# Performance work log

Measured on AMD Instinct MI355X. Metric: run time of the kernel, lower is better.

Reference implementation:

```python
import jax, jax.numpy as jnp
import numpy as np

LN_EPS = 1e-3  # keras LayerNormalization default epsilon


def _layernorm(x, gamma, beta):
    mu = jnp.mean(x, axis=-1, keepdims=True)
    var = jnp.mean(jnp.square(x - mu), axis=-1, keepdims=True)
    return (x - mu) * jax.lax.rsqrt(var + LN_EPS) * gamma + beta


def setup_inputs() -> dict:
    key = jax.random.key(0)
    ks = jax.random.split(key, 8)
    B, H, W, C = 4, 64, 64, 256
    units = 256
    s = 1.0 / np.sqrt(C)  # he-normal-ish scale for 1x1 convs
    return {
        "inputs": jax.random.normal(ks[0], (B, H, W, C), jnp.float32),
        "context": jax.random.normal(ks[1], (B, H, W, C), jnp.float32),
        "Wq": jax.random.normal(ks[2], (C, units), jnp.float32) * s,
        "bq": jnp.zeros((units,), jnp.float32),
        "Wk": jax.random.normal(ks[3], (C, units), jnp.float32) * s,
        "bk": jnp.zeros((units,), jnp.float32),
        "Wv": jax.random.normal(ks[4], (C, units), jnp.float32) * s,
        "bv": jnp.zeros((units,), jnp.float32),
        "Wp": jax.random.normal(ks[5], (units, units), jnp.float32) * s,
        "bp": jnp.zeros((units,), jnp.float32),
        "gamma": jnp.ones((C,), jnp.float32),
        "beta": jnp.zeros((C,), jnp.float32),
    }


def reference(inputs, context, Wq, bq, Wk, bk, Wv, bv, Wp, bp, gamma, beta):
    B, H, W, C = inputs.shape
    units = Wq.shape[1]
    scale = jnp.float32(units) ** -0.5

    x_n = _layernorm(inputs, gamma, beta)          # normalized inputs (also residual base)
    q = jnp.einsum('bhwc,cu->bhwu', x_n, Wq) + bq   # [B,H,W,U]
    k = jnp.einsum('bhwc,cu->bhwu', context, Wk) + bk
    v = jnp.einsum('bhwc,cu->bhwu', context, Wv) + bv

    # full (h*w) x (H*W) score tensor, as in the original
    scores = jnp.einsum('bhwc,bHWc->bhwHW', q, k) * scale
    scores = scores.reshape(B, H, W, H * W)
    attn = jax.nn.softmax(scores, axis=-1).reshape(B, H, W, H, W)

    out = jnp.einsum('bhwHW,bHWc->bhwc', attn, v)
    proj = jnp.einsum('bhwc,cu->bhwu', out, Wp) + bp
    return x_n + proj
```

## Files before the change

kernel.cpp:

```cpp
#include <hip/hip_runtime.h>

typedef short v8s __attribute__((ext_vector_type(8)));
typedef float v4f __attribute__((ext_vector_type(4)));
using u16 = unsigned short;

#define QSCALE 0.09016844f

__device__ __forceinline__ u16 f2b(float f) {
  union { float f; unsigned u; } v; v.f = f;
  unsigned r = v.u + 0x7FFFu + ((v.u >> 16) & 1u);
  return (u16)(r >> 16);
}

__global__ void ln_prep(const float* __restrict__ x, const float* __restrict__ ctx,
                        const float* __restrict__ gamma, const float* __restrict__ beta,
                        float* __restrict__ xn_f, u16* __restrict__ xn_b,
                        u16* __restrict__ ctx_b)
{
  const int tid = threadIdx.x;
  const int wid = tid >> 6, lane = tid & 63;
  const int row = blockIdx.x * 4 + wid;
  const size_t tidx = ((size_t)(row >> 4) * 8 + (lane >> 3)) * 512 +
                      (((lane >> 1) & 3) * 16 + (row & 15)) * 8 + (lane & 1) * 4;
  if (blockIdx.y == 0) {
    const float4 xv = *(const float4*)(x + (size_t)row * 256 + lane * 4);
    float s1 = xv.x + xv.y + xv.z + xv.w;
    float s2 = xv.x*xv.x + xv.y*xv.y + xv.z*xv.z + xv.w*xv.w;
#pragma unroll
    for (int m = 32; m >= 1; m >>= 1) {
      s1 += __shfl_xor(s1, m);
      s2 += __shfl_xor(s2, m);
    }
    const float mu  = s1 * (1.0f/256.0f);
    const float var = s2 * (1.0f/256.0f) - mu*mu;
    const float rs  = rsqrtf(var + 1e-3f);
    const float4 g = *(const float4*)(gamma + lane*4);
    const float4 b = *(const float4*)(beta  + lane*4);
    float4 y;
    y.x = (xv.x-mu)*rs*g.x + b.x;
    y.y = (xv.y-mu)*rs*g.y + b.y;
    y.z = (xv.z-mu)*rs*g.z + b.z;
    y.w = (xv.w-mu)*rs*g.w + b.w;
    *(float4*)(xn_f + (size_t)row*256 + lane*4) = y;
    ushort4 yb; yb.x=f2b(y.x); yb.y=f2b(y.y); yb.z=f2b(y.z); yb.w=f2b(y.w);
    *(ushort4*)(xn_b + tidx) = yb;
  } else {
    const float4 cv = *(const float4*)(ctx + (size_t)row * 256 + lane * 4);
    ushort4 cb; cb.x=f2b(cv.x); cb.y=f2b(cv.y); cb.z=f2b(cv.z); cb.w=f2b(cv.w);
    *(ushort4*)(ctx_b + tidx) = cb;
  }
}

__global__ void wtrans(const float* __restrict__ wq, const float* __restrict__ wk,
                       const float* __restrict__ wv, const float* __restrict__ wp,
                       u16* __restrict__ tq, u16* __restrict__ tk,
                       u16* __restrict__ tv, u16* __restrict__ tp)
{
  const float* src; u16* dst; float scl = 1.0f;
  switch (blockIdx.y) {
    case 0:  src = wq; dst = tq; scl = QSCALE; break;
    case 1:  src = wk; dst = tk; break;
    case 2:  src = wv; dst = tv; break;
    default: src = wp; dst = tp; break;
  }
  const int t  = threadIdx.x;
  const int kk = blockIdx.x * 16 + (t >> 4);
  const int n0 = (t & 15) * 16;
  const size_t base = (size_t)((t & 15) * 8 + (kk >> 5)) * 512 +
                      ((kk >> 3) & 3) * 16 * 8 + (kk & 7);
#pragma unroll
  for (int j = 0; j < 16; j++)
    dst[base + (size_t)j * 8] = f2b(src[(size_t)kk * 256 + n0 + j] * scl);
}

__global__ __launch_bounds__(256) void gemm_qkv(
    const u16* __restrict__ xn_b, const u16* __restrict__ ctx_b,
    const u16* __restrict__ wqt, const u16* __restrict__ wkt, const u16* __restrict__ wvt,
    const float* __restrict__ bq, const float* __restrict__ bk, const float* __restrict__ bv,
    u16* __restrict__ qo, u16* __restrict__ ko, u16* __restrict__ vto)
{
  const int mode = blockIdx.y;
  const u16* A; const u16* Wt; const float* bias;
  if (mode == 0)      { A = xn_b;  Wt = wqt; bias = bq; }
  else if (mode == 1) { A = ctx_b; Wt = wkt; bias = bk; }
  else                { A = ctx_b; Wt = wvt; bias = bv; }
  const float bscale = (mode == 0) ? QSCALE : 1.0f;
  const int wid = threadIdx.x >> 6, lane = threadIdx.x & 63;
  const int lm = lane & 15, q4 = lane >> 4;
  const int m0 = blockIdx.x * 64 + wid * 16;
  const u16* abase = A + (size_t)(m0 >> 4) * 4096 + lane * 8;
  v8s af[8];
#pragma unroll
  for (int kf = 0; kf < 8; kf++) af[kf] = *(const v8s*)(abase + kf * 512);
#pragma unroll
  for (int ct = 0; ct < 16; ct++) {
    const int c = ct * 16 + lm;
    const u16* wbase = Wt + (size_t)ct * 4096 + lane * 8;
    v8s wf[8];
#pragma unroll
    for (int kf = 0; kf < 8; kf++) wf[kf] = *(const v8s*)(wbase + kf * 512);
    v4f a0 = {0.f,0.f,0.f,0.f}, a1 = a0, a2 = a0, a3 = a0;
    a0 = __builtin_amdgcn_mfma_f32_16x16x32_bf16(af[0], wf[0], a0, 0, 0, 0);
    a1 = __builtin_amdgcn_mfma_f32_16x16x32_bf16(af[2], wf[2], a1, 0, 0, 0);
    a2 = __builtin_amdgcn_mfma_f32_16x16x32_bf16(af[4], wf[4], a2, 0, 0, 0);
    a3 = __builtin_amdgcn_mfma_f32_16x16x32_bf16(af[6], wf[6], a3, 0, 0, 0);
    a0 = __builtin_amdgcn_mfma_f32_16x16x32_bf16(af[1], wf[1], a0, 0, 0, 0);
    a1 = __builtin_amdgcn_mfma_f32_16x16x32_bf16(af[3], wf[3], a1, 0, 0, 0);
    a2 = __builtin_amdgcn_mfma_f32_16x16x32_bf16(af[5], wf[5], a2, 0, 0, 0);
    a3 = __builtin_amdgcn_mfma_f32_16x16x32_bf16(af[7], wf[7], a3, 0, 0, 0);
    const v4f acc = (a0 + a1) + (a2 + a3);
    const float bb = bias[c] * bscale;
    if (mode == 2) {
      const int b = m0 >> 12;
      const int chunk = (m0 & 4095) >> 6;
      const int kic = (m0 & 63) + q4 * 4;
      const int ks = kic >> 5;
      const int q4p = (kic >> 3) & 3;
      const size_t idx = ((size_t)(b * 64 + chunk) * 32 + (c >> 4) * 2 + ks) * 512 +
                         (q4p * 16 + (c & 15)) * 8 + (q4 & 1) * 4;
      ushort4 pk;
      pk.x = f2b(acc[0] + bb); pk.y = f2b(acc[1] + bb);
      pk.z = f2b(acc[2] + bb); pk.w = f2b(acc[3] + bb);
      *(ushort4*)(vto + idx) = pk;
    } else {
      u16* out = (mode == 0) ? qo : ko;
      const size_t base = ((size_t)(m0 >> 4) * 8 + (c >> 5)) * 512 +
                          (((c >> 3) & 3) * 16 + q4 * 4) * 8 + (c & 7);
#pragma unroll
      for (int r = 0; r < 4; r++)
        out[base + (size_t)r * 8] = f2b(acc[r] + bb);
    }
  }
}

__global__ __launch_bounds__(512, 2) void attn_kernel(
    const u16* __restrict__ q, const u16* __restrict__ k,
    const u16* __restrict__ vt, u16* __restrict__ ao)
{
  __shared__ u16 P[2][64][136];
  __shared__ float Lp[8][64];
  __shared__ float Lt[64];
  const int bid  = blockIdx.x;
  const int b    = (bid & 7) >> 1;
  const int qblk = ((bid >> 3) << 1) | (bid & 1);
  const int tid  = threadIdx.x;
  const int w    = tid >> 6, lane = tid & 63;
  const int lm   = lane & 15, q4 = lane >> 4;
  const int m0   = qblk * 64;
  const u16* qb = q  + (size_t)b * 1048576;
  const u16* kb = k  + (size_t)b * 1048576;
  const u16* vb = vt + (size_t)b * 1048576;

  v8s qf[4][8];
#pragma unroll
  for (int qt = 0; qt < 4; qt++) {
    const u16* qbase = qb + (size_t)((m0 >> 4) + qt) * 4096 + lane * 8;
#pragma unroll
    for (int kf = 0; kf < 8; kf++) qf[qt][kf] = *(const v8s*)(qbase + kf * 512);
  }

  v4f o[4][2];
#pragma unroll
  for (int qt = 0; qt < 4; qt++)
#pragma unroll
    for (int ct = 0; ct < 2; ct++) o[qt][ct] = (v4f){0.f, 0.f, 0.f, 0.f};
  float lsum[4] = {0.f, 0.f, 0.f, 0.f};

  v8s kfr[8];
  {
    const u16* kbase = kb + (size_t)w * 4096 + lane * 8;
#pragma unroll
    for (int kf = 0; kf < 8; kf++) kfr[kf] = *(const v8s*)(kbase + kf * 512);
  }

  for (int c128 = 0; c128 < 32; c128++) {
    const int pb = c128 & 1;
    v8s vfr[2][4];
#pragma unroll
    for (int ct = 0; ct < 2; ct++)
#pragma unroll
      for (int j = 0; j < 4; j++) {
        const size_t tile = (size_t)(c128 * 2 + (j >> 1)) * 32 +
                            (w * 2 + ct) * 2 + (j & 1);
        vfr[ct][j] = *(const v8s*)(vb + tile * 512 + lane * 8);
      }
    v4f sc[4];
#pragma unroll
    for (int qt = 0; qt < 4; qt++) sc[qt] = (v4f){0.f, 0.f, 0.f, 0.f};
#pragma unroll
    for (int kf = 0; kf < 8; kf++)
#pragma unroll
      for (int qt = 0; qt < 4; qt++)
        sc[qt] = __builtin_amdgcn_mfma_f32_16x16x32_bf16(kfr[kf], qf[qt][kf], sc[qt], 0, 0, 0);
    {
      const int nc = (c128 + 1) & 31;
      const u16* kbase = kb + (size_t)(nc * 8 + w) * 4096 + lane * 8;
#pragma unroll
      for (int kf = 0; kf < 8; kf++) kfr[kf] = *(const v8s*)(kbase + kf * 512);
    }
#pragma unroll
    for (int qt = 0; qt < 4; qt++) {
      const float e0 = exp2f(sc[qt][0]);
      const float e1 = exp2f(sc[qt][1]);
      const float e2 = exp2f(sc[qt][2]);
      const float e3 = exp2f(sc[qt][3]);
      lsum[qt] += (e0 + e1) + (e2 + e3);
      unsigned d0, d1;
      asm("v_cvt_pk_bf16_f32 %0, %1, %2" : "=v"(d0) : "v"(e0), "v"(e1));
      asm("v_cvt_pk_bf16_f32 %0, %1, %2" : "=v"(d1) : "v"(e2), "v"(e3));
      uint2 pk; pk.x = d0; pk.y = d1;
      *(uint2*)(&P[pb][qt * 16 + lm][w * 16 + q4 * 4]) = pk;
    }
    __syncthreads();
#pragma unroll
    for (int qt = 0; qt < 4; qt++) {
      v8s pf[4];
#pragma unroll
      for (int j = 0; j < 4; j++)
        pf[j] = *(const v8s*)(&P[pb][qt * 16 + lm][j * 32 + q4 * 8]);
#pragma unroll
      for (int ct = 0; ct < 2; ct++)
#pragma unroll
        for (int j = 0; j < 4; j++)
          o[qt][ct] = __builtin_amdgcn_mfma_f32_16x16x32_bf16(pf[j], vfr[ct][j], o[qt][ct], 0, 0, 0);
    }
  }

#pragma unroll
  for (int qt = 0; qt < 4; qt++) {
    float t = lsum[qt];
    t += __shfl_xor(t, 16);
    t += __shfl_xor(t, 32);
    lsum[qt] = t;
  }
  if (q4 == 0) {
#pragma unroll
    for (int qt = 0; qt < 4; qt++) Lp[w][qt * 16 + lm] = lsum[qt];
  }
  __syncthreads();
  if (tid < 64) {
    float t = 0.f;
#pragma unroll
    for (int ww = 0; ww < 8; ww++) t += Lp[ww][tid];
    Lt[tid] = t;
  }
  __syncthreads();

  const int rstrip0 = (b * 4096 + m0) >> 4;
#pragma unroll
  for (int qt = 0; qt < 4; qt++)
#pragma unroll
    for (int r = 0; r < 4; r++) {
      const float linv = 1.0f / Lt[qt * 16 + q4 * 4 + r];
#pragma unroll
      for (int ct = 0; ct < 2; ct++) {
        const int ch = w * 32 + ct * 16 + lm;
        const size_t idx = ((size_t)(rstrip0 + qt) * 8 + (ch >> 5)) * 512 +
                           (((ch >> 3) & 3) * 16 + q4 * 4 + r) * 8 + (ch & 7);
        ao[idx] = f2b(o[qt][ct][r] * linv);
      }
    }
}

__global__ __launch_bounds__(256) void gemm_proj(
    const u16* __restrict__ A, const u16* __restrict__ Wt, const float* __restrict__ bias,
    const float* __restrict__ xn_f, float* __restrict__ out)
{
  const int wid = threadIdx.x >> 6, lane = threadIdx.x & 63;
  const int lm = lane & 15, q4 = lane >> 4;
  const int m0 = blockIdx.x * 64 + wid * 16;
  const u16* abase = A + (size_t)(m0 >> 4) * 4096 + lane * 8;
  v8s af[8];
#pragma unroll
  for (int kf = 0; kf < 8; kf++) af[kf] = *(const v8s*)(abase + kf * 512);
#pragma unroll
  for (int ct = 0; ct < 16; ct++) {
    const int c = ct * 16 + lm;
    const u16* wbase = Wt + (size_t)ct * 4096 + lane * 8;
    v8s wf[8];
#pragma unroll
    for (int kf = 0; kf < 8; kf++) wf[kf] = *(const v8s*)(wbase + kf * 512);
    v4f a0 = {0.f,0.f,0.f,0.f}, a1 = a0, a2 = a0, a3 = a0;
    a0 = __builtin_amdgcn_mfma_f32_16x16x32_bf16(af[0], wf[0], a0, 0, 0, 0);
    a1 = __builtin_amdgcn_mfma_f32_16x16x32_bf16(af[2], wf[2], a1, 0, 0, 0);
    a2 = __builtin_amdgcn_mfma_f32_16x16x32_bf16(af[4], wf[4], a2, 0, 0, 0);
    a3 = __builtin_amdgcn_mfma_f32_16x16x32_bf16(af[6], wf[6], a3, 0, 0, 0);
    a0 = __builtin_amdgcn_mfma_f32_16x16x32_bf16(af[1], wf[1], a0, 0, 0, 0);
    a1 = __builtin_amdgcn_mfma_f32_16x16x32_bf16(af[3], wf[3], a1, 0, 0, 0);
    a2 = __builtin_amdgcn_mfma_f32_16x16x32_bf16(af[5], wf[5], a2, 0, 0, 0);
    a3 = __builtin_amdgcn_mfma_f32_16x16x32_bf16(af[7], wf[7], a3, 0, 0, 0);
    const v4f acc = (a0 + a1) + (a2 + a3);
    const float bb = bias[c];
#pragma unroll
    for (int r = 0; r < 4; r++) {
      const size_t idx = (size_t)(m0 + q4 * 4 + r) * 256 + c;
      out[idx] = xn_f[idx] + acc[r] + bb;
    }
  }
}

extern "C" void kernel_launch(void* const* d_in, const int* in_sizes, int n_in,
                              void* d_out, int out_size, void* d_ws, size_t ws_size,
                              hipStream_t stream)
{
  (void)in_sizes; (void)n_in; (void)out_size; (void)ws_size;
  const float* inputs  = (const float*)d_in[0];
  const float* context = (const float*)d_in[1];
  const float* Wq = (const float*)d_in[2];
  const float* bq = (const float*)d_in[3];
  const float* Wk = (const float*)d_in[4];
  const float* bk = (const float*)d_in[5];
  const float* Wv = (const float*)d_in[6];
  const float* bv = (const float*)d_in[7];
  const float* Wp = (const float*)d_in[8];
  const float* bp = (const float*)d_in[9];
  const float* gamma = (const float*)d_in[10];
  const float* beta  = (const float*)d_in[11];
  float* out = (float*)d_out;

  char* p = (char*)d_ws;
  float* xn_f = (float*)p; p += (size_t)16384 * 256 * 4;
  u16* xn_b   = (u16*)p;   p += (size_t)16384 * 256 * 2;
  u16* ctx_b  = (u16*)p;   p += (size_t)16384 * 256 * 2;
  u16* qbuf   = (u16*)p;   p += (size_t)16384 * 256 * 2;
  u16* kbuf   = (u16*)p;   p += (size_t)16384 * 256 * 2;
  u16* vtbuf  = (u16*)p;   p += (size_t)16384 * 256 * 2;
  u16* wqt = (u16*)p; p += (size_t)256 * 256 * 2;
  u16* wkt = (u16*)p; p += (size_t)256 * 256 * 2;
  u16* wvt = (u16*)p; p += (size_t)256 * 256 * 2;
  u16* wpt = (u16*)p; p += (size_t)256 * 256 * 2;
  u16* aobuf = xn_b;

  ln_prep<<<dim3(4096, 2), 256, 0, stream>>>(inputs, context, gamma, beta, xn_f, xn_b, ctx_b);
  wtrans<<<dim3(16, 4), 256, 0, stream>>>(Wq, Wk, Wv, Wp, wqt, wkt, wvt, wpt);
  gemm_qkv<<<dim3(256, 3), 256, 0, stream>>>(xn_b, ctx_b, wqt, wkt, wvt, bq, bk, bv, qbuf, kbuf, vtbuf);
  attn_kernel<<<dim3(256), 512, 0, stream>>>(qbuf, kbuf, vtbuf, aobuf);
  gemm_proj<<<dim3(256), 256, 0, stream>>>(aobuf, wpt, bp, xn_f, out);
}
```

Baseline: 216.7 us.

## Split attention key range across two blocks and merge partials in projection

Each query block's 4096 keys are now split into two halves handled by separate workgroups, doubling the attention grid to 512 blocks. Each half writes a normalized partial output plus its row sums, and the projection GEMM reweights and merges the two partials before the matmul. Launch bounds go from 2 to 4 waves per SIMD to let more blocks co-reside. The aim is better CU occupancy on a grid that previously had only 256 blocks. The cost is extra partial-output traffic, an extra bf16 rounding of the merged output, and possible register pressure or spilling from the tighter launch bound.

```diff
diff --git a/kernel.cpp b/kernel.cpp
--- a/kernel.cpp
+++ b/kernel.cpp
@@ -10,6 +10,10 @@
   union { float f; unsigned u; } v; v.f = f;
   unsigned r = v.u + 0x7FFFu + ((v.u >> 16) & 1u);
   return (u16)(r >> 16);
+}
+__device__ __forceinline__ float b2f(u16 h) {
+  union { unsigned u; float f; } v; v.u = ((unsigned)h) << 16;
+  return v.f;
 }
 
 __global__ void ln_prep(const float* __restrict__ x, const float* __restrict__ ctx,
@@ -133,16 +137,18 @@
   }
 }
 
-__global__ __launch_bounds__(512, 2) void attn_kernel(
+__global__ __launch_bounds__(512, 4) void attn_kernel(
     const u16* __restrict__ q, const u16* __restrict__ k,
-    const u16* __restrict__ vt, u16* __restrict__ ao)
+    const u16* __restrict__ vt, u16* __restrict__ o0, u16* __restrict__ o1,
+    float* __restrict__ Lq)
 {
   __shared__ u16 P[2][64][136];
   __shared__ float Lp[8][64];
   __shared__ float Lt[64];
   const int bid  = blockIdx.x;
   const int b    = (bid & 7) >> 1;
-  const int qblk = ((bid >> 3) << 1) | (bid & 1);
+  const int ks   = bid & 1;
+  const int qblk = bid >> 3;
   const int tid  = threadIdx.x;
   const int w    = tid >> 6, lane = tid & 63;
   const int lm   = lane & 15, q4 = lane >> 4;
@@ -150,6 +156,7 @@
   const u16* qb = q  + (size_t)b * 1048576;
   const u16* kb = k  + (size_t)b * 1048576;
   const u16* vb = vt + (size_t)b * 1048576;
+  const int c0 = ks * 16;
 
   v8s qf[4][8];
 #pragma unroll
@@ -168,12 +175,12 @@
 
   v8s kfr[8];
   {
-    const u16* kbase = kb + (size_t)w * 4096 + lane * 8;
+    const u16* kbase = kb + (size_t)(c0 * 8 + w) * 4096 + lane * 8;
 #pragma unroll
     for (int kf = 0; kf < 8; kf++) kfr[kf] = *(const v8s*)(kbase + kf * 512);
   }
 
-  for (int c128 = 0; c128 < 32; c128++) {
+  for (int c128 = c0; c128 < c0 + 16; c128++) {
     const int pb = c128 & 1;
     v8s vfr[2][4];
 #pragma unroll
@@ -193,7 +200,7 @@
       for (int qt = 0; qt < 4; qt++)
         sc[qt] = __builtin_amdgcn_mfma_f32_16x16x32_bf16(kfr[kf], qf[qt][kf], sc[qt], 0, 0, 0);
     {
-      const int nc = (c128 + 1) & 31;
+      const int nc = c0 + ((c128 + 1 - c0) & 15);
       const u16* kbase = kb + (size_t)(nc * 8 + w) * 4096 + lane * 8;
 #pragma unroll
       for (int kf = 0; kf < 8; kf++) kfr[kf] = *(const v8s*)(kbase + kf * 512);
@@ -243,9 +250,11 @@
 #pragma unroll
     for (int ww = 0; ww < 8; ww++) t += Lp[ww][tid];
     Lt[tid] = t;
+    Lq[ks * 16384 + b * 4096 + m0 + tid] = t;
   }
   __syncthreads();
 
+  u16* od = ks ? o1 : o0;
   const int rstrip0 = (b * 4096 + m0) >> 4;
 #pragma unroll
   for (int qt = 0; qt < 4; qt++)
@@ -257,22 +266,39 @@
         const int ch = w * 32 + ct * 16 + lm;
         const size_t idx = ((size_t)(rstrip0 + qt) * 8 + (ch >> 5)) * 512 +
                            (((ch >> 3) & 3) * 16 + q4 * 4 + r) * 8 + (ch & 7);
-        ao[idx] = f2b(o[qt][ct][r] * linv);
+        od[idx] = f2b(o[qt][ct][r] * linv);
       }
     }
 }
 
 __global__ __launch_bounds__(256) void gemm_proj(
-    const u16* __restrict__ A, const u16* __restrict__ Wt, const float* __restrict__ bias,
+    const u16* __restrict__ o0, const u16* __restrict__ o1,
+    const float* __restrict__ Lq,
+    const u16* __restrict__ Wt, const float* __restrict__ bias,
     const float* __restrict__ xn_f, float* __restrict__ out)
 {
   const int wid = threadIdx.x >> 6, lane = threadIdx.x & 63;
   const int lm = lane & 15, q4 = lane >> 4;
   const int m0 = blockIdx.x * 64 + wid * 16;
-  const u16* abase = A + (size_t)(m0 >> 4) * 4096 + lane * 8;
+  const float l0 = Lq[m0 + lm];
+  const float l1 = Lq[16384 + m0 + lm];
+  const float w0 = l0 / (l0 + l1);
+  const float w1 = 1.0f - w0;
+  const u16* a0base = o0 + (size_t)(m0 >> 4) * 4096 + lane * 8;
+  const u16* a1base = o1 + (size_t)(m0 >> 4) * 4096 + lane * 8;
   v8s af[8];
 #pragma unroll
-  for (int kf = 0; kf < 8; kf++) af[kf] = *(const v8s*)(abase + kf * 512);
+  for (int kf = 0; kf < 8; kf++) {
+    const v8s x0 = *(const v8s*)(a0base + kf * 512);
+    const v8s x1 = *(const v8s*)(a1base + kf * 512);
+    v8s m;
+#pragma unroll
+    for (int e = 0; e < 8; e++) {
+      const float f = w0 * b2f((u16)x0[e]) + w1 * b2f((u16)x1[e]);
+      m[e] = (short)f2b(f);
+    }
+    af[kf] = m;
+  }
 #pragma unroll
   for (int ct = 0; ct < 16; ct++) {
     const int c = ct * 16 + lm;
@@ -329,11 +355,13 @@
   u16* wkt = (u16*)p; p += (size_t)256 * 256 * 2;
   u16* wvt = (u16*)p; p += (size_t)256 * 256 * 2;
   u16* wpt = (u16*)p; p += (size_t)256 * 256 * 2;
-  u16* aobuf = xn_b;
+  float* Lq = (float*)p; p += (size_t)2 * 16384 * 4;
+  u16* o0 = xn_b;
+  u16* o1 = ctx_b;
 
   ln_prep<<<dim3(4096, 2), 256, 0, stream>>>(inputs, context, gamma, beta, xn_f, xn_b, ctx_b);
   wtrans<<<dim3(16, 4), 256, 0, stream>>>(Wq, Wk, Wv, Wp, wqt, wkt, wvt, wpt);
   gemm_qkv<<<dim3(256, 3), 256, 0, stream>>>(xn_b, ctx_b, wqt, wkt, wvt, bq, bk, bv, qbuf, kbuf, vtbuf);
-  attn_kernel<<<dim3(256), 512, 0, stream>>>(qbuf, kbuf, vtbuf, aobuf);
-  gemm_proj<<<dim3(256), 256, 0, stream>>>(aobuf, wpt, bp, xn_f, out);
-}
+  attn_kernel<<<dim3(512), 512, 0, stream>>>(qbuf, kbuf, vtbuf, o0, o1, Lq);
+  gemm_proj<<<dim3(256), 256, 0, stream>>>(o0, o1, Lq, wpt, bp, xn_f, out);
+}
```

After: 504.1 us. 2.33x slower.

## Stage epilogue outputs through LDS for coalesced vector global stores

Applied to the files above, without the earlier changes.

The layernorm/convert kernel now processes 16 rows per block and writes the tiled bf16 layout through a shared-memory buffer, so global stores are 16-byte vectors. The QKV GEMM and the projection GEMM likewise stage their output tiles in LDS and then write them out contiguously. The projection GEMM also reads the residual with float4 loads and uses a swizzle against bank conflicts. This replaces scattered 2-byte and 4-byte global stores, at the cost of extra LDS traffic, a barrier, and larger shared memory (64KB in gemm_proj) that can reduce occupancy.

```diff
diff --git a/kernel.cpp b/kernel.cpp
--- a/kernel.cpp
+++ b/kernel.cpp
@@ -12,42 +12,61 @@
   return (u16)(r >> 16);
 }
 
-__global__ void ln_prep(const float* __restrict__ x, const float* __restrict__ ctx,
-                        const float* __restrict__ gamma, const float* __restrict__ beta,
-                        float* __restrict__ xn_f, u16* __restrict__ xn_b,
-                        u16* __restrict__ ctx_b)
-{
+__global__ __launch_bounds__(256) void ln_prep(
+    const float* __restrict__ x, const float* __restrict__ ctx,
+    const float* __restrict__ gamma, const float* __restrict__ beta,
+    float* __restrict__ xn_f, u16* __restrict__ xn_b, u16* __restrict__ ctx_b)
+{
+  __shared__ u16 Y[16][264];
   const int tid = threadIdx.x;
-  const int wid = tid >> 6, lane = tid & 63;
-  const int row = blockIdx.x * 4 + wid;
-  const size_t tidx = ((size_t)(row >> 4) * 8 + (lane >> 3)) * 512 +
-                      (((lane >> 1) & 3) * 16 + (row & 15)) * 8 + (lane & 1) * 4;
+  const int w = tid >> 6, lane = tid & 63;
+  const int rowg0 = blockIdx.x * 16;
   if (blockIdx.y == 0) {
-    const float4 xv = *(const float4*)(x + (size_t)row * 256 + lane * 4);
-    float s1 = xv.x + xv.y + xv.z + xv.w;
-    float s2 = xv.x*xv.x + xv.y*xv.y + xv.z*xv.z + xv.w*xv.w;
-#pragma unroll
-    for (int m = 32; m >= 1; m >>= 1) {
-      s1 += __shfl_xor(s1, m);
-      s2 += __shfl_xor(s2, m);
-    }
-    const float mu  = s1 * (1.0f/256.0f);
-    const float var = s2 * (1.0f/256.0f) - mu*mu;
-    const float rs  = rsqrtf(var + 1e-3f);
     const float4 g = *(const float4*)(gamma + lane*4);
     const float4 b = *(const float4*)(beta  + lane*4);
-    float4 y;
-    y.x = (xv.x-mu)*rs*g.x + b.x;
-    y.y = (xv.y-mu)*rs*g.y + b.y;
-    y.z = (xv.z-mu)*rs*g.z + b.z;
-    y.w = (xv.w-mu)*rs*g.w + b.w;
-    *(float4*)(xn_f + (size_t)row*256 + lane*4) = y;
-    ushort4 yb; yb.x=f2b(y.x); yb.y=f2b(y.y); yb.z=f2b(y.z); yb.w=f2b(y.w);
-    *(ushort4*)(xn_b + tidx) = yb;
+#pragma unroll
+    for (int rr = 0; rr < 4; rr++) {
+      const int r16 = w * 4 + rr;
+      const int row = rowg0 + r16;
+      const float4 xv = *(const float4*)(x + (size_t)row * 256 + lane * 4);
+      float s1 = xv.x + xv.y + xv.z + xv.w;
+      float s2 = xv.x*xv.x + xv.y*xv.y + xv.z*xv.z + xv.w*xv.w;
+#pragma unroll
+      for (int m = 32; m >= 1; m >>= 1) {
+        s1 += __shfl_xor(s1, m);
+        s2 += __shfl_xor(s2, m);
+      }
+      const float mu  = s1 * (1.0f/256.0f);
+      const float var = s2 * (1.0f/256.0f) - mu*mu;
+      const float rs  = rsqrtf(var + 1e-3f);
+      float4 y;
+      y.x = (xv.x-mu)*rs*g.x + b.x;
+      y.y = (xv.y-mu)*rs*g.y + b.y;
+      y.z = (xv.z-mu)*rs*g.z + b.z;
+      y.w = (xv.w-mu)*rs*g.w + b.w;
+      *(float4*)(xn_f + (size_t)row*256 + lane*4) = y;
+      ushort4 yb; yb.x=f2b(y.x); yb.y=f2b(y.y); yb.z=f2b(y.z); yb.w=f2b(y.w);
+      *(ushort4*)(&Y[r16][lane*4]) = yb;
+    }
   } else {
-    const float4 cv = *(const float4*)(ctx + (size_t)row * 256 + lane * 4);
-    ushort4 cb; cb.x=f2b(cv.x); cb.y=f2b(cv.y); cb.z=f2b(cv.z); cb.w=f2b(cv.w);
-    *(ushort4*)(ctx_b + tidx) = cb;
+#pragma unroll
+    for (int rr = 0; rr < 4; rr++) {
+      const int r16 = w * 4 + rr;
+      const int row = rowg0 + r16;
+      const float4 cv = *(const float4*)(ctx + (size_t)row * 256 + lane * 4);
+      ushort4 cb; cb.x=f2b(cv.x); cb.y=f2b(cv.y); cb.z=f2b(cv.z); cb.w=f2b(cv.w);
+      *(ushort4*)(&Y[r16][lane*4]) = cb;
+    }
+  }
+  __syncthreads();
+  u16* dst = (blockIdx.y == 0 ? xn_b : ctx_b) + (size_t)blockIdx.x * 4096;
+#pragma unroll
+  for (int j = 0; j < 2; j++) {
+    const int o8  = tid + j * 256;
+    const int sub = o8 >> 6, within = o8 & 63;
+    const int row = within & 15, chq = within >> 4;
+    const int ch  = sub * 32 + chq * 8;
+    *(v8s*)(dst + (size_t)o8 * 8) = *(const v8s*)(&Y[row][ch]);
   }
 }
 
@@ -79,6 +98,7 @@
     const float* __restrict__ bq, const float* __restrict__ bk, const float* __restrict__ bv,
     u16* __restrict__ qo, u16* __restrict__ ko, u16* __restrict__ vto)
 {
+  __shared__ u16 Cb[16384];
   const int mode = blockIdx.y;
   const u16* A; const u16* Wt; const float* bias;
   if (mode == 0)      { A = xn_b;  Wt = wqt; bias = bq; }
@@ -87,7 +107,8 @@
   const float bscale = (mode == 0) ? QSCALE : 1.0f;
   const int wid = threadIdx.x >> 6, lane = threadIdx.x & 63;
   const int lm = lane & 15, q4 = lane >> 4;
-  const int m0 = blockIdx.x * 64 + wid * 16;
+  const int m0b = blockIdx.x * 64;
+  const int m0 = m0b + wid * 16;
   const u16* abase = A + (size_t)(m0 >> 4) * 4096 + lane * 8;
   v8s af[8];
 #pragma unroll
@@ -111,25 +132,33 @@
     const v4f acc = (a0 + a1) + (a2 + a3);
     const float bb = bias[c] * bscale;
     if (mode == 2) {
-      const int b = m0 >> 12;
-      const int chunk = (m0 & 4095) >> 6;
       const int kic = (m0 & 63) + q4 * 4;
-      const int ks = kic >> 5;
+      const int ks  = kic >> 5;
       const int q4p = (kic >> 3) & 3;
-      const size_t idx = ((size_t)(b * 64 + chunk) * 32 + (c >> 4) * 2 + ks) * 512 +
-                         (q4p * 16 + (c & 15)) * 8 + (q4 & 1) * 4;
+      const int lidx = ((c >> 4) * 2 + ks) * 512 + (q4p * 16 + (c & 15)) * 8 + (q4 & 1) * 4;
       ushort4 pk;
       pk.x = f2b(acc[0] + bb); pk.y = f2b(acc[1] + bb);
       pk.z = f2b(acc[2] + bb); pk.w = f2b(acc[3] + bb);
-      *(ushort4*)(vto + idx) = pk;
+      *(ushort4*)(&Cb[lidx]) = pk;
     } else {
-      u16* out = (mode == 0) ? qo : ko;
-      const size_t base = ((size_t)(m0 >> 4) * 8 + (c >> 5)) * 512 +
-                          (((c >> 3) & 3) * 16 + q4 * 4) * 8 + (c & 7);
-#pragma unroll
-      for (int r = 0; r < 4; r++)
-        out[base + (size_t)r * 8] = f2b(acc[r] + bb);
-    }
+      const int lidx = wid * 4096 + (c >> 5) * 512 +
+                       (((c >> 3) & 3) * 16 + q4 * 4) * 8 + (c & 7);
+#pragma unroll
+      for (int r = 0; r < 4; r++) Cb[lidx + r * 8] = f2b(acc[r] + bb);
+    }
+  }
+  __syncthreads();
+  u16* gdst;
+  if (mode == 2) {
+    const int b = m0b >> 12, chunk = (m0b & 4095) >> 6;
+    gdst = vto + (size_t)(b * 64 + chunk) * 16384;
+  } else {
+    gdst = (mode == 0 ? qo : ko) + (size_t)(m0b >> 4) * 4096;
+  }
+#pragma unroll
+  for (int j = 0; j < 8; j++) {
+    const int o8 = threadIdx.x + j * 256;
+    *(v8s*)(gdst + (size_t)o8 * 8) = *(const v8s*)(&Cb[o8 * 8]);
   }
 }
 
@@ -266,9 +295,11 @@
     const u16* __restrict__ A, const u16* __restrict__ Wt, const float* __restrict__ bias,
     const float* __restrict__ xn_f, float* __restrict__ out)
 {
+  __shared__ float Cf[64][256];
   const int wid = threadIdx.x >> 6, lane = threadIdx.x & 63;
   const int lm = lane & 15, q4 = lane >> 4;
-  const int m0 = blockIdx.x * 64 + wid * 16;
+  const int m0b = blockIdx.x * 64;
+  const int m0 = m0b + wid * 16;
   const u16* abase = A + (size_t)(m0 >> 4) * 4096 + lane * 8;
   v8s af[8];
 #pragma unroll
@@ -293,9 +324,25 @@
     const float bb = bias[c];
 #pragma unroll
     for (int r = 0; r < 4; r++) {
-      const size_t idx = (size_t)(m0 + q4 * 4 + r) * 256 + c;
-      out[idx] = xn_f[idx] + acc[r] + bb;
-    }
+      const int row = wid * 16 + q4 * 4 + r;
+      Cf[row][c ^ (q4 * 8)] = acc[r] + bb;
+    }
+  }
+  __syncthreads();
+  const float* xb = xn_f + (size_t)m0b * 256;
+  float* ob = out + (size_t)m0b * 256;
+#pragma unroll
+  for (int j = 0; j < 16; j++) {
+    const int u = threadIdx.x + j * 256;
+    const int row = u >> 6;
+    const int c = (u & 63) * 4;
+    const int csw = c ^ (((row >> 2) & 3) * 8);
+    const float4 a4 = *(const float4*)(&Cf[row][csw]);
+    const float4 x4 = *(const float4*)(xb + (size_t)row * 256 + c);
+    float4 o4;
+    o4.x = a4.x + x4.x; o4.y = a4.y + x4.y;
+    o4.z = a4.z + x4.z; o4.w = a4.w + x4.w;
+    *(float4*)(ob + (size_t)row * 256 + c) = o4;
   }
 }
 
@@ -331,7 +378,7 @@
   u16* wpt = (u16*)p; p += (size_t)256 * 256 * 2;
   u16* aobuf = xn_b;
 
-  ln_prep<<<dim3(4096, 2), 256, 0, stream>>>(inputs, context, gamma, beta, xn_f, xn_b, ctx_b);
+  ln_prep<<<dim3(1024, 2), 256, 0, stream>>>(inputs, context, gamma, beta, xn_f, xn_b, ctx_b);
   wtrans<<<dim3(16, 4), 256, 0, stream>>>(Wq, Wk, Wv, Wp, wqt, wkt, wvt, wpt);
   gemm_qkv<<<dim3(256, 3), 256, 0, stream>>>(xn_b, ctx_b, wqt, wkt, wvt, bq, bk, bv, qbuf, kbuf, vtbuf);
   attn_kernel<<<dim3(256), 512, 0, stream>>>(qbuf, kbuf, vtbuf, aobuf);
```

Result: no change. 212.7 us (-1.8%).

## Fuse layernorm into QKV GEMM and output projection into attention kernel

Applied to the files above, without the earlier changes.

Removes the separate ln_prep and gemm_proj kernels. LayerNorm and the bf16 conversion of the context now run inside gemm_qkv, which stages the rows through shared memory. The attention output goes through LDS straight into the projection MFMA, adding bias and residual in the same kernel. QKV outputs are also staged in LDS and written as coalesced 16-byte stores. This cuts two launches and the bf16 intermediate round trips through global memory. In exchange, context is now read and converted twice (K and V blocks), and the attention kernel carries a longer epilogue with more register and LDS use.

```diff
diff --git a/kernel.cpp b/kernel.cpp
--- a/kernel.cpp
+++ b/kernel.cpp
@@ -10,45 +10,6 @@
   union { float f; unsigned u; } v; v.f = f;
   unsigned r = v.u + 0x7FFFu + ((v.u >> 16) & 1u);
   return (u16)(r >> 16);
-}
-
-__global__ void ln_prep(const float* __restrict__ x, const float* __restrict__ ctx,
-                        const float* __restrict__ gamma, const float* __restrict__ beta,
-                        float* __restrict__ xn_f, u16* __restrict__ xn_b,
-                        u16* __restrict__ ctx_b)
-{
-  const int tid = threadIdx.x;
-  const int wid = tid >> 6, lane = tid & 63;
-  const int row = blockIdx.x * 4 + wid;
-  const size_t tidx = ((size_t)(row >> 4) * 8 + (lane >> 3)) * 512 +
-                      (((lane >> 1) & 3) * 16 + (row & 15)) * 8 + (lane & 1) * 4;
-  if (blockIdx.y == 0) {
-    const float4 xv = *(const float4*)(x + (size_t)row * 256 + lane * 4);
-    float s1 = xv.x + xv.y + xv.z + xv.w;
-    float s2 = xv.x*xv.x + xv.y*xv.y + xv.z*xv.z + xv.w*xv.w;
-#pragma unroll
-    for (int m = 32; m >= 1; m >>= 1) {
-      s1 += __shfl_xor(s1, m);
-      s2 += __shfl_xor(s2, m);
-    }
-    const float mu  = s1 * (1.0f/256.0f);
-    const float var = s2 * (1.0f/256.0f) - mu*mu;
-    const float rs  = rsqrtf(var + 1e-3f);
-    const float4 g = *(const float4*)(gamma + lane*4);
-    const float4 b = *(const float4*)(beta  + lane*4);
-    float4 y;
-    y.x = (xv.x-mu)*rs*g.x + b.x;
-    y.y = (xv.y-mu)*rs*g.y + b.y;
-    y.z = (xv.z-mu)*rs*g.z + b.z;
-    y.w = (xv.w-mu)*rs*g.w + b.w;
-    *(float4*)(xn_f + (size_t)row*256 + lane*4) = y;
-    ushort4 yb; yb.x=f2b(y.x); yb.y=f2b(y.y); yb.z=f2b(y.z); yb.w=f2b(y.w);
-    *(ushort4*)(xn_b + tidx) = yb;
-  } else {
-    const float4 cv = *(const float4*)(ctx + (size_t)row * 256 + lane * 4);
-    ushort4 cb; cb.x=f2b(cv.x); cb.y=f2b(cv.y); cb.z=f2b(cv.z); cb.w=f2b(cv.w);
-    *(ushort4*)(ctx_b + tidx) = cb;
-  }
 }
 
 __global__ void wtrans(const float* __restrict__ wq, const float* __restrict__ wk,
@@ -74,24 +35,72 @@
 }
 
 __global__ __launch_bounds__(256) void gemm_qkv(
-    const u16* __restrict__ xn_b, const u16* __restrict__ ctx_b,
+    const float* __restrict__ x, const float* __restrict__ ctx,
+    const float* __restrict__ gamma, const float* __restrict__ beta,
     const u16* __restrict__ wqt, const u16* __restrict__ wkt, const u16* __restrict__ wvt,
     const float* __restrict__ bq, const float* __restrict__ bk, const float* __restrict__ bv,
-    u16* __restrict__ qo, u16* __restrict__ ko, u16* __restrict__ vto)
+    float* __restrict__ xn_f, u16* __restrict__ qo, u16* __restrict__ ko,
+    u16* __restrict__ vto)
 {
+  __shared__ union {
+    u16 Y[64][264];
+    u16 Cb[16384];
+  } S;
   const int mode = blockIdx.y;
-  const u16* A; const u16* Wt; const float* bias;
-  if (mode == 0)      { A = xn_b;  Wt = wqt; bias = bq; }
-  else if (mode == 1) { A = ctx_b; Wt = wkt; bias = bk; }
-  else                { A = ctx_b; Wt = wvt; bias = bv; }
-  const float bscale = (mode == 0) ? QSCALE : 1.0f;
   const int wid = threadIdx.x >> 6, lane = threadIdx.x & 63;
   const int lm = lane & 15, q4 = lane >> 4;
-  const int m0 = blockIdx.x * 64 + wid * 16;
-  const u16* abase = A + (size_t)(m0 >> 4) * 4096 + lane * 8;
+  const int m0b = blockIdx.x * 64;
+
+  if (mode == 0) {
+    const float4 g = *(const float4*)(gamma + lane * 4);
+    const float4 bt = *(const float4*)(beta + lane * 4);
+#pragma unroll
+    for (int i = 0; i < 16; i++) {
+      const int rb = wid * 16 + i;
+      const int row = m0b + rb;
+      const float4 xv = *(const float4*)(x + (size_t)row * 256 + lane * 4);
+      float s1 = xv.x + xv.y + xv.z + xv.w;
+      float s2 = xv.x*xv.x + xv.y*xv.y + xv.z*xv.z + xv.w*xv.w;
+#pragma unroll
+      for (int m = 32; m >= 1; m >>= 1) {
+        s1 += __shfl_xor(s1, m);
+        s2 += __shfl_xor(s2, m);
+      }
+      const float mu  = s1 * (1.0f/256.0f);
+      const float var = s2 * (1.0f/256.0f) - mu*mu;
+      const float rs  = rsqrtf(var + 1e-3f);
+      float4 y;
+      y.x = (xv.x-mu)*rs*g.x + bt.x;
+      y.y = (xv.y-mu)*rs*g.y + bt.y;
+      y.z = (xv.z-mu)*rs*g.z + bt.z;
+      y.w = (xv.w-mu)*rs*g.w + bt.w;
+      *(float4*)(xn_f + (size_t)row * 256 + lane * 4) = y;
+      ushort4 yb; yb.x=f2b(y.x); yb.y=f2b(y.y); yb.z=f2b(y.z); yb.w=f2b(y.w);
+      *(ushort4*)(&S.Y[rb][lane * 4]) = yb;
+    }
+  } else {
+#pragma unroll
+    for (int i = 0; i < 16; i++) {
+      const int rb = wid * 16 + i;
+      const float4 cv = *(const float4*)(ctx + (size_t)(m0b + rb) * 256 + lane * 4);
+      ushort4 cb; cb.x=f2b(cv.x); cb.y=f2b(cv.y); cb.z=f2b(cv.z); cb.w=f2b(cv.w);
+      *(ushort4*)(&S.Y[rb][lane * 4]) = cb;
+    }
+  }
+  __syncthreads();
+
   v8s af[8];
 #pragma unroll
-  for (int kf = 0; kf < 8; kf++) af[kf] = *(const v8s*)(abase + kf * 512);
+  for (int kf = 0; kf < 8; kf++)
+    af[kf] = *(const v8s*)(&S.Y[wid * 16 + lm][kf * 32 + q4 * 8]);
+  __syncthreads();
+
+  const u16* Wt; const float* bias;
+  if (mode == 0)      { Wt = wqt; bias = bq; }
+  else if (mode == 1) { Wt = wkt; bias = bk; }
+  else                { Wt = wvt; bias = bv; }
+  const float bscale = (mode == 0) ? QSCALE : 1.0f;
+
 #pragma unroll
   for (int ct = 0; ct < 16; ct++) {
     const int c = ct * 16 + lm;
@@ -111,33 +120,46 @@
     const v4f acc = (a0 + a1) + (a2 + a3);
     const float bb = bias[c] * bscale;
     if (mode == 2) {
-      const int b = m0 >> 12;
-      const int chunk = (m0 & 4095) >> 6;
-      const int kic = (m0 & 63) + q4 * 4;
-      const int ks = kic >> 5;
+      const int kic = wid * 16 + q4 * 4;
+      const int ks  = kic >> 5;
       const int q4p = (kic >> 3) & 3;
-      const size_t idx = ((size_t)(b * 64 + chunk) * 32 + (c >> 4) * 2 + ks) * 512 +
-                         (q4p * 16 + (c & 15)) * 8 + (q4 & 1) * 4;
+      const int lidx = ((c >> 4) * 2 + ks) * 512 + (q4p * 16 + (c & 15)) * 8 + (q4 & 1) * 4;
       ushort4 pk;
       pk.x = f2b(acc[0] + bb); pk.y = f2b(acc[1] + bb);
       pk.z = f2b(acc[2] + bb); pk.w = f2b(acc[3] + bb);
-      *(ushort4*)(vto + idx) = pk;
+      *(ushort4*)(&S.Cb[lidx]) = pk;
     } else {
-      u16* out = (mode == 0) ? qo : ko;
-      const size_t base = ((size_t)(m0 >> 4) * 8 + (c >> 5)) * 512 +
-                          (((c >> 3) & 3) * 16 + q4 * 4) * 8 + (c & 7);
-#pragma unroll
-      for (int r = 0; r < 4; r++)
-        out[base + (size_t)r * 8] = f2b(acc[r] + bb);
-    }
+      const int lidx = wid * 4096 + (c >> 5) * 512 +
+                       (((c >> 3) & 3) * 16 + q4 * 4) * 8 + (c & 7);
+#pragma unroll
+      for (int r = 0; r < 4; r++) S.Cb[lidx + r * 8] = f2b(acc[r] + bb);
+    }
+  }
+  __syncthreads();
+  u16* gdst;
+  if (mode == 2) {
+    const int b = m0b >> 12, chunk = (m0b & 4095) >> 6;
+    gdst = vto + (size_t)(b * 64 + chunk) * 16384;
+  } else {
+    gdst = (mode == 0 ? qo : ko) + (size_t)(m0b >> 4) * 4096;
+  }
+#pragma unroll
+  for (int j = 0; j < 8; j++) {
+    const int o8 = threadIdx.x + j * 256;
+    *(v8s*)(gdst + (size_t)o8 * 8) = *(const v8s*)(&S.Cb[o8 * 8]);
   }
 }
 
 __global__ __launch_bounds__(512, 2) void attn_kernel(
     const u16* __restrict__ q, const u16* __restrict__ k,
-    const u16* __restrict__ vt, u16* __restrict__ ao)
+    const u16* __restrict__ vt, const u16* __restrict__ wpt,
+    const float* __restrict__ bp, const float* __restrict__ xn_f,
+    float* __restrict__ out)
 {
-  __shared__ u16 P[2][64][136];
+  __shared__ union {
+    u16 P[2][64][136];
+    u16 Yt[64][264];
+  } S;
   __shared__ float Lp[8][64];
   __shared__ float Lt[64];
   const int bid  = blockIdx.x;
@@ -209,7 +231,7 @@
       asm("v_cvt_pk_bf16_f32 %0, %1, %2" : "=v"(d0) : "v"(e0), "v"(e1));
       asm("v_cvt_pk_bf16_f32 %0, %1, %2" : "=v"(d1) : "v"(e2), "v"(e3));
       uint2 pk; pk.x = d0; pk.y = d1;
-      *(uint2*)(&P[pb][qt * 16 + lm][w * 16 + q4 * 4]) = pk;
+      *(uint2*)(&S.P[pb][qt * 16 + lm][w * 16 + q4 * 4]) = pk;
     }
     __syncthreads();
 #pragma unroll
@@ -217,7 +239,7 @@
       v8s pf[4];
 #pragma unroll
       for (int j = 0; j < 4; j++)
-        pf[j] = *(const v8s*)(&P[pb][qt * 16 + lm][j * 32 + q4 * 8]);
+        pf[j] = *(const v8s*)(&S.P[pb][qt * 16 + lm][j * 32 + q4 * 8]);
 #pragma unroll
       for (int ct = 0; ct < 2; ct++)
 #pragma unroll
@@ -246,7 +268,6 @@
   }
   __syncthreads();
 
-  const int rstrip0 = (b * 4096 + m0) >> 4;
 #pragma unroll
   for (int qt = 0; qt < 4; qt++)
 #pragma unroll
@@ -255,46 +276,40 @@
 #pragma unroll
       for (int ct = 0; ct < 2; ct++) {
         const int ch = w * 32 + ct * 16 + lm;
-        const size_t idx = ((size_t)(rstrip0 + qt) * 8 + (ch >> 5)) * 512 +
-                           (((ch >> 3) & 3) * 16 + q4 * 4 + r) * 8 + (ch & 7);
-        ao[idx] = f2b(o[qt][ct][r] * linv);
+        S.Yt[qt * 16 + q4 * 4 + r][ch] = f2b(o[qt][ct][r] * linv);
       }
     }
-}
-
-__global__ __launch_bounds__(256) void gemm_proj(
-    const u16* __restrict__ A, const u16* __restrict__ Wt, const float* __restrict__ bias,
-    const float* __restrict__ xn_f, float* __restrict__ out)
-{
-  const int wid = threadIdx.x >> 6, lane = threadIdx.x & 63;
-  const int lm = lane & 15, q4 = lane >> 4;
-  const int m0 = blockIdx.x * 64 + wid * 16;
-  const u16* abase = A + (size_t)(m0 >> 4) * 4096 + lane * 8;
-  v8s af[8];
-#pragma unroll
-  for (int kf = 0; kf < 8; kf++) af[kf] = *(const v8s*)(abase + kf * 512);
-#pragma unroll
-  for (int ct = 0; ct < 16; ct++) {
+  __syncthreads();
+  const int s = w >> 1, h = w & 1;
+  v8s paf[8];
+#pragma unroll
+  for (int kf = 0; kf < 8; kf++)
+    paf[kf] = *(const v8s*)(&S.Yt[s * 16 + lm][kf * 32 + q4 * 8]);
+  const float* xb = xn_f + (size_t)(b * 4096 + m0) * 256;
+  float* ob = out + (size_t)(b * 4096 + m0) * 256;
+#pragma unroll
+  for (int ctl = 0; ctl < 8; ctl++) {
+    const int ct = h * 8 + ctl;
     const int c = ct * 16 + lm;
-    const u16* wbase = Wt + (size_t)ct * 4096 + lane * 8;
+    const u16* wbase = wpt + (size_t)ct * 4096 + lane * 8;
     v8s wf[8];
 #pragma unroll
     for (int kf = 0; kf < 8; kf++) wf[kf] = *(const v8s*)(wbase + kf * 512);
     v4f a0 = {0.f,0.f,0.f,0.f}, a1 = a0, a2 = a0, a3 = a0;
-    a0 = __builtin_amdgcn_mfma_f32_16x16x32_bf16(af[0], wf[0], a0, 0, 0, 0);
-    a1 = __builtin_amdgcn_mfma_f32_16x16x32_bf16(af[2], wf[2], a1, 0, 0, 0);
-    a2 = __builtin_amdgcn_mfma_f32_16x16x32_bf16(af[4], wf[4], a2, 0, 0, 0);
-    a3 = __builtin_amdgcn_mfma_f32_16x16x32_bf16(af[6], wf[6], a3, 0, 0, 0);
-    a0 = __builtin_amdgcn_mfma_f32_16x16x32_bf16(af[1], wf[1], a0, 0, 0, 0);
-    a1 = __builtin_amdgcn_mfma_f32_16x16x32_bf16(af[3], wf[3], a1, 0, 0, 0);
-    a2 = __builtin_amdgcn_mfma_f32_16x16x32_bf16(af[5], wf[5], a2, 0, 0, 0);
-    a3 = __builtin_amdgcn_mfma_f32_16x16x32_bf16(af[7], wf[7], a3, 0, 0, 0);
+    a0 = __builtin_amdgcn_mfma_f32_16x16x32_bf16(paf[0], wf[0], a0, 0, 0, 0);
+    a1 = __builtin_amdgcn_mfma_f32_16x16x32_bf16(paf[2], wf[2], a1, 0, 0, 0);
+    a2 = __builtin_amdgcn_mfma_f32_16x16x32_bf16(paf[4], wf[4], a2, 0, 0, 0);
+    a3 = __builtin_amdgcn_mfma_f32_16x16x32_bf16(paf[6], wf[6], a3, 0, 0, 0);
+    a0 = __builtin_amdgcn_mfma_f32_16x16x32_bf16(paf[1], wf[1], a0, 0, 0, 0);
+    a1 = __builtin_amdgcn_mfma_f32_16x16x32_bf16(paf[3], wf[3], a1, 0, 0, 0);
+    a2 = __builtin_amdgcn_mfma_f32_16x16x32_bf16(paf[5], wf[5], a2, 0, 0, 0);
+    a3 = __builtin_amdgcn_mfma_f32_16x16x32_bf16(paf[7], wf[7], a3, 0, 0, 0);
     const v4f acc = (a0 + a1) + (a2 + a3);
-    const float bb = bias[c];
+    const float bb = bp[c];
 #pragma unroll
     for (int r = 0; r < 4; r++) {
-      const size_t idx = (size_t)(m0 + q4 * 4 + r) * 256 + c;
-      out[idx] = xn_f[idx] + acc[r] + bb;
+      const size_t idx = (size_t)(s * 16 + q4 * 4 + r) * 256 + c;
+      ob[idx] = xb[idx] + acc[r] + bb;
     }
   }
 }
@@ -320,8 +335,6 @@
 
   char* p = (char*)d_ws;
   float* xn_f = (float*)p; p += (size_t)16384 * 256 * 4;
-  u16* xn_b   = (u16*)p;   p += (size_t)16384 * 256 * 2;
-  u16* ctx_b  = (u16*)p;   p += (size_t)16384 * 256 * 2;
   u16* qbuf   = (u16*)p;   p += (size_t)16384 * 256 * 2;
   u16* kbuf   = (u16*)p;   p += (size_t)16384 * 256 * 2;
   u16* vtbuf  = (u16*)p;   p += (size_t)16384 * 256 * 2;
@@ -329,11 +342,10 @@
   u16* wkt = (u16*)p; p += (size_t)256 * 256 * 2;
   u16* wvt = (u16*)p; p += (size_t)256 * 256 * 2;
   u16* wpt = (u16*)p; p += (size_t)256 * 256 * 2;
-  u16* aobuf = xn_b;
-
-  ln_prep<<<dim3(4096, 2), 256, 0, stream>>>(inputs, context, gamma, beta, xn_f, xn_b, ctx_b);
+
   wtrans<<<dim3(16, 4), 256, 0, stream>>>(Wq, Wk, Wv, Wp, wqt, wkt, wvt, wpt);
-  gemm_qkv<<<dim3(256, 3), 256, 0, stream>>>(xn_b, ctx_b, wqt, wkt, wvt, bq, bk, bv, qbuf, kbuf, vtbuf);
-  attn_kernel<<<dim3(256), 512, 0, stream>>>(qbuf, kbuf, vtbuf, aobuf);
-  gemm_proj<<<dim3(256), 256, 0, stream>>>(aobuf, wpt, bp, xn_f, out);
-}
+  gemm_qkv<<<dim3(256, 3), 256, 0, stream>>>(inputs, context, gamma, beta,
+                                             wqt, wkt, wvt, bq, bk, bv,
+                                             xn_f, qbuf, kbuf, vtbuf);
+  attn_kernel<<<dim3(256), 512, 0, stream>>>(qbuf, kbuf, vtbuf, wpt, bp, xn_f, out);
+}
```

Result: faster. 209.3 us (-3.4%).
